# Performance work log

Measured on AMD Instinct MI355X. Metric: run time of the kernel, lower is better.

## Reference

```python
import jax, jax.numpy as jnp
import numpy as np

ROUTINGS = 3

def squash(s, axis):
    # squash(s) = (|s|^2/(1+|s|^2)) * s/|s|
    n2 = jnp.sum(s * s, axis=axis, keepdims=True)
    return (n2 / (1.0 + n2)) * s * jax.lax.rsqrt(n2 + 1e-8)

def setup_inputs() -> dict:
    key = jax.random.key(0)
    k1, k2 = jax.random.split(key)
    B0, B1, C, H, W = 2, 4, 64, 32, 32
    K, S, pad = 3, 8, 1
    x = jax.random.normal(k1, (B0, B1, C, H, W), dtype=jnp.float32)
    stdv = 1.0 / np.sqrt(C * K * K)
    weight = jax.random.uniform(k2, (1, 1, C, K * K, 1, S), dtype=jnp.float32,
                                minval=-stdv, maxval=stdv)
    # im2col gather indices into flattened padded (H+2p)*(W+2p) map, k-major order
    Wp = W + 2 * pad
    base = (np.arange(H)[:, None] * Wp + np.arange(W)[None, :]).ravel()      # (P,)
    offs = (np.arange(K)[:, None] * Wp + np.arange(K)[None, :]).ravel()      # (k_len,)
    indexm = jnp.asarray((offs[:, None] + base[None, :]).ravel(), dtype=jnp.int32)
    return {"x": x, "weight": weight, "indexm": indexm, "padding": pad}

def reference(x, weight, indexm, padding):
    B0, B1, C, H, W = x.shape
    k_len, set_num = weight.shape[3], weight.shape[5]
    p = int(padding)
    xp = jnp.pad(x, ((0, 0), (0, 0), (0, 0), (p, p), (p, p)))
    xf = xp.reshape(B0, B1, C, -1)
    g = jnp.take(xf, indexm, axis=-1)                      # (B0,B1,C,k_len*P)
    u = g.reshape(B0, B1, C, k_len, -1, 1) * weight        # (B0,B1,C,k_len,P,S)
    u_hat = jnp.transpose(u, (1, 3, 0, 2, 4, 5)).reshape(B1 * k_len, -1, set_num)
    # dynamic routing; retain_grad=False -> routing uses stop_gradient copy
    u_r = jax.lax.stop_gradient(u_hat)
    c = jnp.full((1, 1, set_num), 1.0 / set_num, dtype=x.dtype)
    for _ in range(ROUTINGS - 1):
        v = squash(jnp.sum(u_r * c, axis=1), axis=1)       # (N1, S)
        b = u_r * v[:, None, :]                            # (N1, N2, S)
        c = jax.nn.softmax(b, axis=2)
    v = squash(jnp.sum(u_hat * c, axis=1), axis=1)
    return v[:, None, :] / 2.0 + 0.5                       # (B1*k_len, 1, S)
```

## Files before the change

### kernel.cpp

```cpp
#include <hip/hip_runtime.h>

#define B0_   2
#define B1_   4
#define C_    64
#define HH    32
#define WW    32
#define P_    1024
#define KLEN  9
#define S_    8
#define N1_   36
#define WP    34
#define SPLIT 16
#define BCPB  8
#define THREADS 256

__device__ __forceinline__ void block_reduce_store(float acc[8], int n1, int split,
                                                   float* __restrict__ out) {
    __shared__ float red[4][8];
    int tid = threadIdx.x;
    int lane = tid & 63, wid = tid >> 6;
#pragma unroll
    for (int s = 0; s < 8; ++s) {
        float v = acc[s];
#pragma unroll
        for (int off = 32; off >= 1; off >>= 1) v += __shfl_down(v, off, 64);
        if (lane == 0) red[wid][s] = v;
    }
    __syncthreads();
    if (tid < 8) {
        float t = red[0][tid] + red[1][tid] + red[2][tid] + red[3][tid];
        out[(n1 * SPLIT + split) * 8 + tid] = t;
    }
}

__device__ __forceinline__ void decode_offsets(const int* __restrict__ indexm,
                                               int k, int tid, int offhw[4]) {
#pragma unroll
    for (int j = 0; j < 4; ++j) {
        int p = tid + j * THREADS;
        int idx = indexm[k * P_ + p];
        int r  = idx / WP;
        int cc = idx - r * WP;
        int ir = r - 1, ic = cc - 1;
        offhw[j] = (ir >= 0 && ir < HH && ic >= 0 && ic < WW) ? ir * WW + ic : -1;
    }
}

__global__ __launch_bounds__(THREADS)
void pass_uniform(const float* __restrict__ x, const float* __restrict__ wgt,
                  const int* __restrict__ indexm, float* __restrict__ partOut) {
    int split = blockIdx.x;
    int n1 = blockIdx.y;
    int tid = threadIdx.x;
    int k = n1 % KLEN, b1 = n1 / KLEN;

    int offhw[4];
    decode_offsets(indexm, k, tid, offhw);

    float acc[8] = {0.f,0.f,0.f,0.f,0.f,0.f,0.f,0.f};
    for (int bc = split * BCPB; bc < split * BCPB + BCPB; ++bc) {
        int b0 = bc >> 6, c = bc & 63;
        const float* xc = x + ((((b0 << 2) + b1) << 6) + c) * P_;
        const float* wc = wgt + c * (KLEN * S_) + k * S_;
        float w[8];
#pragma unroll
        for (int s = 0; s < 8; ++s) w[s] = wc[s];
#pragma unroll
        for (int j = 0; j < 4; ++j) {
            float g = (offhw[j] >= 0) ? xc[offhw[j]] : 0.f;
#pragma unroll
            for (int s = 0; s < 8; ++s) acc[s] += g * w[s];
        }
    }
    block_reduce_store(acc, n1, split, partOut);
}

__global__ __launch_bounds__(THREADS)
void pass_route(const float* __restrict__ x, const float* __restrict__ wgt,
                const int* __restrict__ indexm, const float* __restrict__ partPrev,
                float prevScale, float* __restrict__ partOut) {
    int split = blockIdx.x;
    int n1 = blockIdx.y;
    int tid = threadIdx.x;
    int k = n1 % KLEN, b1 = n1 / KLEN;

    float vp[8] = {0.f,0.f,0.f,0.f,0.f,0.f,0.f,0.f};
#pragma unroll
    for (int i = 0; i < SPLIT; ++i) {
        const float* pp = partPrev + (n1 * SPLIT + i) * 8;
#pragma unroll
        for (int s = 0; s < 8; ++s) vp[s] += pp[s];
    }
    float n2 = 0.f;
#pragma unroll
    for (int s = 0; s < 8; ++s) { vp[s] *= prevScale; n2 += vp[s] * vp[s]; }
    float f = (n2 / (1.f + n2)) * rsqrtf(n2 + 1e-8f);
#pragma unroll
    for (int s = 0; s < 8; ++s) vp[s] *= f;

    int offhw[4];
    decode_offsets(indexm, k, tid, offhw);

    float acc[8] = {0.f,0.f,0.f,0.f,0.f,0.f,0.f,0.f};
    for (int bc = split * BCPB; bc < split * BCPB + BCPB; ++bc) {
        int b0 = bc >> 6, c = bc & 63;
        const float* xc = x + ((((b0 << 2) + b1) << 6) + c) * P_;
        const float* wc = wgt + c * (KLEN * S_) + k * S_;
        float w[8], wv[8];
#pragma unroll
        for (int s = 0; s < 8; ++s) { w[s] = wc[s]; wv[s] = w[s] * vp[s]; }
#pragma unroll
        for (int j = 0; j < 4; ++j) {
            float g = (offhw[j] >= 0) ? xc[offhw[j]] : 0.f;
            float e[8]; float Z = 0.f;
#pragma unroll
            for (int s = 0; s < 8; ++s) { e[s] = __expf(g * wv[s]); Z += e[s]; }
            float sc = g * __builtin_amdgcn_rcpf(Z);
#pragma unroll
            for (int s = 0; s < 8; ++s) acc[s] += sc * w[s] * e[s];
        }
    }
    block_reduce_store(acc, n1, split, partOut);
}

__global__ void finalize_out(const float* __restrict__ part3, float* __restrict__ out) {
    int tid = threadIdx.x;
    if (tid < N1_) {
        float v[8] = {0.f,0.f,0.f,0.f,0.f,0.f,0.f,0.f};
#pragma unroll
        for (int i = 0; i < SPLIT; ++i) {
            const float* pp = part3 + (tid * SPLIT + i) * 8;
#pragma unroll
            for (int s = 0; s < 8; ++s) v[s] += pp[s];
        }
        float n2 = 0.f;
#pragma unroll
        for (int s = 0; s < 8; ++s) n2 += v[s] * v[s];
        float f = (n2 / (1.f + n2)) * rsqrtf(n2 + 1e-8f);
#pragma unroll
        for (int s = 0; s < 8; ++s) out[tid * 8 + s] = v[s] * f * 0.5f + 0.5f;
    }
}

extern "C" void kernel_launch(void* const* d_in, const int* in_sizes, int n_in,
                              void* d_out, int out_size, void* d_ws, size_t ws_size,
                              hipStream_t stream) {
    const float* x    = (const float*)d_in[0];
    const float* wgt  = (const float*)d_in[1];
    const int*   idxm = (const int*)d_in[2];
    float* ws = (float*)d_ws;
    const int PBANK = N1_ * SPLIT * S_;
    float* P1 = ws;
    float* P2 = ws + PBANK;
    float* P3 = ws + 2 * PBANK;

    dim3 grid(SPLIT, N1_);
    pass_uniform<<<grid, THREADS, 0, stream>>>(x, wgt, idxm, P1);
    pass_route <<<grid, THREADS, 0, stream>>>(x, wgt, idxm, P1, 0.125f, P2);
    pass_route <<<grid, THREADS, 0, stream>>>(x, wgt, idxm, P2, 1.0f,   P3);
    finalize_out<<<1, 64, 0, stream>>>(P3, (float*)d_out);
}
```

Before: 41.56 us.

## Fuse routing passes into one persistent kernel with grid barriers

Replaces the four separate launches (uniform pass, two routing passes, finalize) with a control-reset kernel plus one fused kernel. The fused kernel uses atomic grid barriers between routing iterations and a last-block-per-capsule counter to do the final squash. This is meant to remove kernel launch gaps and the separate finalize launch, and it also keeps gather offsets in registers across phases. It relies on all 576 blocks being co-resident (launch bounds set to 4 blocks per SM), otherwise the spin barrier deadlocks. It also switches exp to exp2 with a pre-scaled log2e factor.

Result: slower. 117.4 us (+182.5%).

```diff
diff --git a/kernel.cpp b/kernel.cpp
--- a/kernel.cpp
+++ b/kernel.cpp
@@ -1,22 +1,48 @@
 #include <hip/hip_runtime.h>
 
-#define B0_   2
-#define B1_   4
-#define C_    64
-#define HH    32
-#define WW    32
 #define P_    1024
 #define KLEN  9
 #define S_    8
 #define N1_   36
 #define WP    34
+#define HH    32
+#define WW    32
 #define SPLIT 16
 #define BCPB  8
 #define THREADS 256
-
-__device__ __forceinline__ void block_reduce_store(float acc[8], int n1, int split,
-                                                   float* __restrict__ out) {
-    __shared__ float red[4][8];
+#define NBLK  (N1_ * SPLIT)
+#define LOG2E 1.4426950408889634f
+
+#define PBANK    (N1_ * SPLIT * S_)
+#define CTRL_OFF (3 * PBANK)
+#define NCTRL    (2 + N1_)
+
+struct SharedBufs {
+    float red[4][8];
+    float vsh[8];
+    int   last;
+};
+
+__device__ __forceinline__ float agent_loadf(const float* p) {
+    return __hip_atomic_load(p, __ATOMIC_RELAXED, __HIP_MEMORY_SCOPE_AGENT);
+}
+__device__ __forceinline__ void agent_storef(float* p, float v) {
+    __hip_atomic_store(p, v, __ATOMIC_RELAXED, __HIP_MEMORY_SCOPE_AGENT);
+}
+
+__device__ __forceinline__ void grid_barrier(unsigned* cnt) {
+    __syncthreads();
+    if (threadIdx.x == 0) {
+        __hip_atomic_fetch_add(cnt, 1u, __ATOMIC_ACQ_REL, __HIP_MEMORY_SCOPE_AGENT);
+        while (__hip_atomic_load(cnt, __ATOMIC_ACQUIRE, __HIP_MEMORY_SCOPE_AGENT)
+               < (unsigned)NBLK)
+            __builtin_amdgcn_s_sleep(8);
+    }
+    __syncthreads();
+}
+
+__device__ __forceinline__ void block_reduce_store(SharedBufs& sh, float acc[8],
+                                                   int slot, float* __restrict__ out) {
     int tid = threadIdx.x;
     int lane = tid & 63, wid = tid >> 6;
 #pragma unroll
@@ -24,121 +50,161 @@
         float v = acc[s];
 #pragma unroll
         for (int off = 32; off >= 1; off >>= 1) v += __shfl_down(v, off, 64);
-        if (lane == 0) red[wid][s] = v;
+        if (lane == 0) sh.red[wid][s] = v;
     }
     __syncthreads();
     if (tid < 8) {
-        float t = red[0][tid] + red[1][tid] + red[2][tid] + red[3][tid];
-        out[(n1 * SPLIT + split) * 8 + tid] = t;
-    }
-}
-
-__device__ __forceinline__ void decode_offsets(const int* __restrict__ indexm,
-                                               int k, int tid, int offhw[4]) {
+        float t = sh.red[0][tid] + sh.red[1][tid] + sh.red[2][tid] + sh.red[3][tid];
+        agent_storef(&out[slot * 8 + tid], t);
+    }
+}
+
+__device__ __forceinline__ void load_squash(SharedBufs& sh, const float* __restrict__ part,
+                                            int n1, float scale, float vp[8]) {
+    int tid = threadIdx.x;
+    if (tid < 8) {
+        float v = 0.f;
+#pragma unroll
+        for (int i = 0; i < SPLIT; ++i) v += agent_loadf(&part[(n1 * SPLIT + i) * 8 + tid]);
+        sh.vsh[tid] = v;
+    }
+    __syncthreads();
+    float n2 = 0.f;
+#pragma unroll
+    for (int s = 0; s < 8; ++s) { vp[s] = sh.vsh[s] * scale; n2 += vp[s] * vp[s]; }
+    float f = (n2 / (1.f + n2)) * rsqrtf(n2 + 1e-8f);
+#pragma unroll
+    for (int s = 0; s < 8; ++s) vp[s] *= f;
+    __syncthreads();
+}
+
+__device__ __forceinline__ float gather_g(const float* __restrict__ x, int b1, int bc,
+                                          const int offhw[4], int j) {
+    int b0 = bc >> 6, c = bc & 63;
+    const float* xc = x + ((((b0 << 2) + b1) << 6) + c) * P_;
+    return (offhw[j] >= 0) ? xc[offhw[j]] : 0.f;
+}
+
+__device__ __forceinline__ void route_acc(const float* __restrict__ x,
+                                          const float* __restrict__ wgt,
+                                          int b1, int k, int bc0, const int offhw[4],
+                                          const float vp[8], float acc[8]) {
+    for (int i = 0; i < BCPB; ++i) {
+        int bc = bc0 + i;
+        int c = bc & 63;
+        const float* wc = wgt + c * (KLEN * S_) + k * S_;
+        float w[8], wv[8];
+#pragma unroll
+        for (int s = 0; s < 8; ++s) { w[s] = wc[s]; wv[s] = w[s] * vp[s] * LOG2E; }
+#pragma unroll
+        for (int j = 0; j < 4; ++j) {
+            float g = gather_g(x, b1, bc, offhw, j);
+            float e[8]; float Z = 0.f;
+#pragma unroll
+            for (int s = 0; s < 8; ++s) { e[s] = __builtin_amdgcn_exp2f(g * wv[s]); Z += e[s]; }
+            float sc = g * __builtin_amdgcn_rcpf(Z);
+#pragma unroll
+            for (int s = 0; s < 8; ++s) acc[s] += sc * w[s] * e[s];
+        }
+    }
+}
+
+__global__ void init_ctrl(unsigned* __restrict__ ctrl) {
+    int t = threadIdx.x;
+    if (t < NCTRL)
+        __hip_atomic_store(&ctrl[t], 0u, __ATOMIC_RELAXED, __HIP_MEMORY_SCOPE_AGENT);
+}
+
+__global__ __launch_bounds__(THREADS, 4)
+void cap_all(const float* __restrict__ x, const float* __restrict__ wgt,
+             const int* __restrict__ indexm, float* __restrict__ ws,
+             float* __restrict__ out)
+{
+    __shared__ SharedBufs sh;
+    float* P1 = ws;
+    float* P2 = ws + PBANK;
+    float* P3 = ws + 2 * PBANK;
+    unsigned* ctrl = (unsigned*)(ws + CTRL_OFF);
+    unsigned* bar  = ctrl;
+    unsigned* done = ctrl + 2;
+
+    const int bid   = blockIdx.x;
+    const int split = bid & (SPLIT - 1);
+    const int n1    = bid >> 4;
+    const int tid   = threadIdx.x;
+    const int k = n1 % KLEN, b1 = n1 / KLEN;
+    const int bc0 = split * BCPB;
+
+    int offhw[4];
 #pragma unroll
     for (int j = 0; j < 4; ++j) {
         int p = tid + j * THREADS;
         int idx = indexm[k * P_ + p];
-        int r  = idx / WP;
-        int cc = idx - r * WP;
+        int r = idx / WP, cc = idx - r * WP;
         int ir = r - 1, ic = cc - 1;
         offhw[j] = (ir >= 0 && ir < HH && ic >= 0 && ic < WW) ? ir * WW + ic : -1;
     }
-}
-
-__global__ __launch_bounds__(THREADS)
-void pass_uniform(const float* __restrict__ x, const float* __restrict__ wgt,
-                  const int* __restrict__ indexm, float* __restrict__ partOut) {
-    int split = blockIdx.x;
-    int n1 = blockIdx.y;
-    int tid = threadIdx.x;
-    int k = n1 % KLEN, b1 = n1 / KLEN;
-
-    int offhw[4];
-    decode_offsets(indexm, k, tid, offhw);
-
-    float acc[8] = {0.f,0.f,0.f,0.f,0.f,0.f,0.f,0.f};
-    for (int bc = split * BCPB; bc < split * BCPB + BCPB; ++bc) {
-        int b0 = bc >> 6, c = bc & 63;
-        const float* xc = x + ((((b0 << 2) + b1) << 6) + c) * P_;
-        const float* wc = wgt + c * (KLEN * S_) + k * S_;
-        float w[8];
-#pragma unroll
-        for (int s = 0; s < 8; ++s) w[s] = wc[s];
-#pragma unroll
-        for (int j = 0; j < 4; ++j) {
-            float g = (offhw[j] >= 0) ? xc[offhw[j]] : 0.f;
-#pragma unroll
-            for (int s = 0; s < 8; ++s) acc[s] += g * w[s];
-        }
-    }
-    block_reduce_store(acc, n1, split, partOut);
-}
-
-__global__ __launch_bounds__(THREADS)
-void pass_route(const float* __restrict__ x, const float* __restrict__ wgt,
-                const int* __restrict__ indexm, const float* __restrict__ partPrev,
-                float prevScale, float* __restrict__ partOut) {
-    int split = blockIdx.x;
-    int n1 = blockIdx.y;
-    int tid = threadIdx.x;
-    int k = n1 % KLEN, b1 = n1 / KLEN;
-
-    float vp[8] = {0.f,0.f,0.f,0.f,0.f,0.f,0.f,0.f};
-#pragma unroll
-    for (int i = 0; i < SPLIT; ++i) {
-        const float* pp = partPrev + (n1 * SPLIT + i) * 8;
-#pragma unroll
-        for (int s = 0; s < 8; ++s) vp[s] += pp[s];
-    }
-    float n2 = 0.f;
-#pragma unroll
-    for (int s = 0; s < 8; ++s) { vp[s] *= prevScale; n2 += vp[s] * vp[s]; }
-    float f = (n2 / (1.f + n2)) * rsqrtf(n2 + 1e-8f);
-#pragma unroll
-    for (int s = 0; s < 8; ++s) vp[s] *= f;
-
-    int offhw[4];
-    decode_offsets(indexm, k, tid, offhw);
-
-    float acc[8] = {0.f,0.f,0.f,0.f,0.f,0.f,0.f,0.f};
-    for (int bc = split * BCPB; bc < split * BCPB + BCPB; ++bc) {
-        int b0 = bc >> 6, c = bc & 63;
-        const float* xc = x + ((((b0 << 2) + b1) << 6) + c) * P_;
-        const float* wc = wgt + c * (KLEN * S_) + k * S_;
-        float w[8], wv[8];
-#pragma unroll
-        for (int s = 0; s < 8; ++s) { w[s] = wc[s]; wv[s] = w[s] * vp[s]; }
-#pragma unroll
-        for (int j = 0; j < 4; ++j) {
-            float g = (offhw[j] >= 0) ? xc[offhw[j]] : 0.f;
-            float e[8]; float Z = 0.f;
-#pragma unroll
-            for (int s = 0; s < 8; ++s) { e[s] = __expf(g * wv[s]); Z += e[s]; }
-            float sc = g * __builtin_amdgcn_rcpf(Z);
-#pragma unroll
-            for (int s = 0; s < 8; ++s) acc[s] += sc * w[s] * e[s];
-        }
-    }
-    block_reduce_store(acc, n1, split, partOut);
-}
-
-__global__ void finalize_out(const float* __restrict__ part3, float* __restrict__ out) {
-    int tid = threadIdx.x;
-    if (tid < N1_) {
-        float v[8] = {0.f,0.f,0.f,0.f,0.f,0.f,0.f,0.f};
-#pragma unroll
-        for (int i = 0; i < SPLIT; ++i) {
-            const float* pp = part3 + (tid * SPLIT + i) * 8;
-#pragma unroll
-            for (int s = 0; s < 8; ++s) v[s] += pp[s];
-        }
-        float n2 = 0.f;
-#pragma unroll
-        for (int s = 0; s < 8; ++s) n2 += v[s] * v[s];
-        float f = (n2 / (1.f + n2)) * rsqrtf(n2 + 1e-8f);
-#pragma unroll
-        for (int s = 0; s < 8; ++s) out[tid * 8 + s] = v[s] * f * 0.5f + 0.5f;
+
+    {
+        float acc[8] = {0.f,0.f,0.f,0.f,0.f,0.f,0.f,0.f};
+        for (int i = 0; i < BCPB; ++i) {
+            int bc = bc0 + i;
+            int c = bc & 63;
+            const float* wc = wgt + c * (KLEN * S_) + k * S_;
+            float w[8];
+#pragma unroll
+            for (int s = 0; s < 8; ++s) w[s] = wc[s];
+#pragma unroll
+            for (int j = 0; j < 4; ++j) {
+                float g = gather_g(x, b1, bc, offhw, j);
+#pragma unroll
+                for (int s = 0; s < 8; ++s) acc[s] += g * w[s];
+            }
+        }
+        block_reduce_store(sh, acc, bid, P1);
+    }
+    grid_barrier(&bar[0]);
+
+    {
+        float vp[8];
+        load_squash(sh, P1, n1, 0.125f, vp);
+        float acc[8] = {0.f,0.f,0.f,0.f,0.f,0.f,0.f,0.f};
+        route_acc(x, wgt, b1, k, bc0, offhw, vp, acc);
+        block_reduce_store(sh, acc, bid, P2);
+    }
+    grid_barrier(&bar[1]);
+
+    {
+        float vp[8];
+        load_squash(sh, P2, n1, 1.0f, vp);
+        float acc[8] = {0.f,0.f,0.f,0.f,0.f,0.f,0.f,0.f};
+        route_acc(x, wgt, b1, k, bc0, offhw, vp, acc);
+        block_reduce_store(sh, acc, bid, P3);
+    }
+
+    __syncthreads();
+    if (tid == 0) {
+        unsigned old = __hip_atomic_fetch_add(&done[n1], 1u, __ATOMIC_ACQ_REL,
+                                              __HIP_MEMORY_SCOPE_AGENT);
+        sh.last = (old == SPLIT - 1);
+    }
+    __syncthreads();
+    if (sh.last) {
+        if (tid < 8) {
+            float v = 0.f;
+#pragma unroll
+            for (int i = 0; i < SPLIT; ++i)
+                v += agent_loadf(&P3[(n1 * SPLIT + i) * 8 + tid]);
+            sh.vsh[tid] = v;
+        }
+        __syncthreads();
+        if (tid < 8) {
+            float n2 = 0.f;
+#pragma unroll
+            for (int s = 0; s < 8; ++s) n2 += sh.vsh[s] * sh.vsh[s];
+            float f = (n2 / (1.f + n2)) * rsqrtf(n2 + 1e-8f);
+            out[n1 * 8 + tid] = sh.vsh[tid] * f * 0.5f + 0.5f;
+        }
     }
 }
 
@@ -149,14 +215,8 @@
     const float* wgt  = (const float*)d_in[1];
     const int*   idxm = (const int*)d_in[2];
     float* ws = (float*)d_ws;
-    const int PBANK = N1_ * SPLIT * S_;
-    float* P1 = ws;
-    float* P2 = ws + PBANK;
-    float* P3 = ws + 2 * PBANK;
-
-    dim3 grid(SPLIT, N1_);
-    pass_uniform<<<grid, THREADS, 0, stream>>>(x, wgt, idxm, P1);
-    pass_route <<<grid, THREADS, 0, stream>>>(x, wgt, idxm, P1, 0.125f, P2);
-    pass_route <<<grid, THREADS, 0, stream>>>(x, wgt, idxm, P2, 1.0f,   P3);
-    finalize_out<<<1, 64, 0, stream>>>(P3, (float*)d_out);
-}
+    unsigned* ctrl = (unsigned*)(ws + CTRL_OFF);
+
+    init_ctrl<<<1, 64, 0, stream>>>(ctrl);
+    cap_all<<<NBLK, THREADS, 0, stream>>>(x, wgt, idxm, ws, (float*)d_out);
+}
```
